# Kernel tuning notes

Measured on AMD Instinct MI355X. Metric: run time of the kernel, lower is better.

Reference implementation:

```python
import jax, jax.numpy as jnp
import numpy as np

N, E, DIN, DH = 50000, 1600000, 128, 128
P_DROP = 0.5


def setup_inputs() -> dict:
    key = jax.random.key(0)
    ks = jax.random.split(key, 9)
    scale = 0.05
    x = jax.random.normal(ks[0], (N, DIN), jnp.float32)
    edge_index = jax.random.randint(ks[1], (2, E), 0, N, dtype=jnp.int32)
    W0 = jax.random.normal(ks[2], (DH, DIN), jnp.float32) * scale
    b0 = jnp.zeros((DH,), jnp.float32)
    W1 = jax.random.normal(ks[3], (DH, DH), jnp.float32) * scale
    b1 = jnp.zeros((DH,), jnp.float32)
    W2 = jax.random.normal(ks[4], (DH, DH), jnp.float32) * scale
    b2 = jnp.zeros((DH,), jnp.float32)
    # deterministic inverted-dropout mask (train-mode Dropout(p=0.5))
    drop_mask = jax.random.bernoulli(ks[5], 1.0 - P_DROP, (N, DH)).astype(jnp.float32) / (1.0 - P_DROP)
    return {"x": x, "edge_index": edge_index, "drop_mask": drop_mask,
            "W0": W0, "b0": b0, "W1": W1, "b1": b1, "W2": W2, "b2": b2}


def _gcn_conv(h_in, W, b, src, dst, dinv):
    # PyG GCNConv: linear -> symmetric-normalized aggregation with self loops -> bias
    h = h_in @ W.T                                   # [N, out]
    norm = dinv[src] * dinv[dst]                      # [E]
    msg = h[src] * norm[:, None]                      # [E, out]
    out = jax.ops.segment_sum(msg, dst, num_segments=N)
    out = out + h * (dinv * dinv)[:, None]            # self-loop contribution
    return out + b


def reference(x, edge_index, drop_mask, W0, b0, W1, b1, W2, b2):
    src, dst = edge_index[0], edge_index[1]
    # degree of target nodes, +1 for the added self loop (shared by all layers)
    deg = jax.ops.segment_sum(jnp.ones((E,), x.dtype), dst, num_segments=N) + 1.0
    dinv = jax.lax.rsqrt(deg)

    h = _gcn_conv(x, W0, b0, src, dst, dinv)
    h = jax.nn.relu(h * drop_mask)                    # Dropout(0.5) then ReLU
    x_ = _gcn_conv(h, W1, b1, src, dst, dinv)
    x2 = _gcn_conv(h, W2, b2, src, dst, dinv)         # conv2 also consumes h (as in source)
    return (x_, x2)
```

## Files before the change

kernel.cpp:

```cpp
#include <hip/hip_runtime.h>


#define D 128
#define BK_SHIFT 7
#define BK_NODES 128
#define NBMAX 512
#define BUFCAP 6144
#define TILE_A 2048
#define TILE_CH 4096

typedef __attribute__((ext_vector_type(8))) short bf16x8;
typedef __attribute__((ext_vector_type(4))) float f32x4;

static __device__ __forceinline__ unsigned f2bf(float f) {
  union { float f; unsigned u; } v; v.f = f;
  unsigned r = v.u + 0x7FFF + ((v.u >> 16) & 1);
  return r >> 16;
}
static __device__ __forceinline__ float bflo(unsigned u) {
  return __uint_as_float(u << 16);
}
static __device__ __forceinline__ float bfhi(unsigned u) {
  return __uint_as_float(u & 0xFFFF0000u);
}


__global__ __launch_bounds__(256) void k_chist(const int* __restrict__ dst,
                                               int* __restrict__ coarse,
                                               int E, int nb) {
  __shared__ int bins[NBMAX];
  int t = threadIdx.x;
  int e0 = blockIdx.x * TILE_CH;
  for (int b = t; b < nb; b += 256) bins[b] = 0;
  __syncthreads();
  for (int i = t; i < TILE_CH; i += 256) {
    int e = e0 + i;
    if (e < E) atomicAdd(&bins[dst[e] >> BK_SHIFT], 1);
  }
  __syncthreads();
  for (int b = t; b < nb; b += 256) {
    int v = bins[b];
    if (v) atomicAdd(&coarse[b], v);
  }
}

__global__ __launch_bounds__(NBMAX) void k_cscan(const int* __restrict__ coarse,
                                                 int* __restrict__ cbase,
                                                 int* __restrict__ bCursor,
                                                 int nb, int E) {
  __shared__ int sm[NBMAX];
  int t = threadIdx.x;
  int v = (t < nb) ? coarse[t] : 0;
  sm[t] = v;
  __syncthreads();
  for (int off = 1; off < NBMAX; off <<= 1) {
    int y = (t >= off) ? sm[t - off] : 0;
    __syncthreads();
    sm[t] += y;
    __syncthreads();
  }
  int excl = sm[t] - v;
  if (t < nb) { cbase[t] = excl; bCursor[t] = excl; }
  if (t == 0) cbase[nb] = E;
}

__global__ __launch_bounds__(256) void k_bucketA(const int* __restrict__ src,
                                                 const int* __restrict__ dst,
                                                 int* __restrict__ bCursor,
                                                 int* __restrict__ packed,
                                                 int E, int nb) {
  __shared__ int hist[NBMAX];
  __shared__ int base[NBMAX];
  int t = threadIdx.x;
  int e0 = blockIdx.x * TILE_A;

  for (int b = t; b < nb; b += 256) hist[b] = 0;
  __syncthreads();

  for (int i = t; i < TILE_A; i += 256) {
    int e = e0 + i;
    if (e < E) atomicAdd(&hist[dst[e] >> BK_SHIFT], 1);
  }
  __syncthreads();

  for (int b = t; b < nb; b += 256) {
    int h = hist[b];
    if (h) base[b] = atomicAdd(&bCursor[b], h);
  }
  __syncthreads();

  for (int i = t; i < TILE_A; i += 256) {
    int e = e0 + i;
    if (e < E) {
      int d = dst[e];
      int bkt = d >> BK_SHIFT;
      int pos = atomicAdd(&base[bkt], 1);
      packed[pos] = (src[e] & 0xFFFF) | ((d & (BK_NODES - 1)) << 16);
    }
  }
}

__global__ __launch_bounds__(512) void k_bucketB2(const int* __restrict__ packed,
                                                  const int* __restrict__ cbase,
                                                  int* __restrict__ srcSorted,
                                                  int* __restrict__ rowptr,
                                                  float* __restrict__ dinv,
                                                  int n, int E) {
  __shared__ int histC[BK_NODES];
  __shared__ int cur[BK_NODES];
  __shared__ int buf[BUFCAP];
  int t = threadIdx.x;
  int bkt = blockIdx.x;
  int n0 = bkt << BK_SHIFT;
  int beg = cbase[bkt], end = cbase[bkt + 1];
  int cnt = end - beg;

  if (t < BK_NODES) histC[t] = 0;
  __syncthreads();

  for (int i = t; i < cnt; i += 512)
    atomicAdd(&histC[packed[beg + i] >> 16], 1);
  __syncthreads();

  if (t == 0) {
    int run = 0;
#pragma unroll
    for (int j = 0; j < BK_NODES; ++j) { cur[j] = run; run += histC[j]; }
  }
  __syncthreads();

  if (t < BK_NODES && n0 + t < n) {
    rowptr[n0 + t] = beg + cur[t];
    dinv[n0 + t]   = rsqrtf((float)histC[t] + 1.0f);
  }
  if (bkt == (int)gridDim.x - 1 && t == 0) rowptr[n] = E;
  __syncthreads();

  if (cnt <= BUFCAP) {
    for (int i = t; i < cnt; i += 512) {
      int p = packed[beg + i];
      int pos = atomicAdd(&cur[p >> 16], 1);
      buf[pos] = p & 0xFFFF;
    }
    __syncthreads();
    for (int i = t; i < cnt; i += 512) srcSorted[beg + i] = buf[i];
  } else {
    for (int i = t; i < cnt; i += 512) {
      int p = packed[beg + i];
      int pos = atomicAdd(&cur[p >> 16], 1);
      srcSorted[beg + pos] = p & 0xFFFF;
    }
  }
}


template <int EPI>
__global__ __launch_bounds__(256) void k_aggb(const unsigned* __restrict__ T,
                                              const int* __restrict__ srcSorted,
                                              const int* __restrict__ rowptr,
                                              const float* __restrict__ dinv,
                                              const float* __restrict__ bias,
                                              const float* __restrict__ mask,
                                              float* __restrict__ outF,
                                              unsigned* __restrict__ outB,
                                              int n) {
  int wave = (blockIdx.x * 256 + threadIdx.x) >> 6;
  int lane = threadIdx.x & 63;
  if (wave >= n) return;
  int beg = rowptr[wave], end = rowptr[wave + 1];
  float ax = 0.f, ay = 0.f, bx = 0.f, by = 0.f;
  int j = beg;
  for (; j + 7 < end; j += 8) {
    int s0 = srcSorted[j],     s1 = srcSorted[j + 1];
    int s2 = srcSorted[j + 2], s3 = srcSorted[j + 3];
    int s4 = srcSorted[j + 4], s5 = srcSorted[j + 5];
    int s6 = srcSorted[j + 6], s7 = srcSorted[j + 7];
    unsigned u0 = T[(size_t)s0 * 64 + lane];
    unsigned u1 = T[(size_t)s1 * 64 + lane];
    unsigned u2 = T[(size_t)s2 * 64 + lane];
    unsigned u3 = T[(size_t)s3 * 64 + lane];
    unsigned u4 = T[(size_t)s4 * 64 + lane];
    unsigned u5 = T[(size_t)s5 * 64 + lane];
    unsigned u6 = T[(size_t)s6 * 64 + lane];
    unsigned u7 = T[(size_t)s7 * 64 + lane];
    ax += bflo(u0) + bflo(u2);  bx += bflo(u1) + bflo(u3);
    ay += bfhi(u0) + bfhi(u2);  by += bfhi(u1) + bfhi(u3);
    ax += bflo(u4) + bflo(u6);  bx += bflo(u5) + bflo(u7);
    ay += bfhi(u4) + bfhi(u6);  by += bfhi(u5) + bfhi(u7);
  }
  for (; j < end; ++j) {
    int s = srcSorted[j];
    unsigned u = T[(size_t)s * 64 + lane];
    ax += bflo(u);
    ay += bfhi(u);
  }
  unsigned us = T[(size_t)wave * 64 + lane];
  float dn = dinv[wave];
  float ox = (ax + bx + bflo(us)) * dn;
  float oy = (ay + by + bfhi(us)) * dn;
  if (EPI == 1) {
    float2 bv = ((const float2*)bias)[lane];
    float2 mv = ((const float2*)mask)[(size_t)wave * 64 + lane];
    float hx = fmaxf((ox + bv.x) * mv.x, 0.f);
    float hy = fmaxf((oy + bv.y) * mv.y, 0.f);
    outB[(size_t)wave * 64 + lane] = f2bf(hx * dn) | (f2bf(hy * dn) << 16);
  } else if (EPI == 2) {
    outB[(size_t)wave * 64 + lane] = f2bf(ox) | (f2bf(oy) << 16);
  } else {
    ((float2*)outF)[(size_t)wave * 64 + lane] = make_float2(ox, oy);
  }
}


__global__ __launch_bounds__(256) void k_wcvt(const float* __restrict__ W0,
                                              const float* __restrict__ W1,
                                              const float* __restrict__ W2,
                                              unsigned short* __restrict__ out) {
  int i = blockIdx.x * 256 + threadIdx.x;
  if (i >= 3 * 16384) return;
  const float* W = (i < 16384) ? W0 : (i < 32768 ? W1 : W2);
  out[i] = (unsigned short)f2bf(W[i & 16383]);
}


template <bool BF16IN, bool BF16OUT>
__global__ __launch_bounds__(256) void k_gemm_mfma(const void* __restrict__ Xv,
                                                   const unsigned short* __restrict__ Wb,
                                                   const float* __restrict__ bias,
                                                   const float* __restrict__ prescale,
                                                   float* __restrict__ Cf,
                                                   unsigned short* __restrict__ Cb,
                                                   int nrows) {
  int wid  = threadIdx.x >> 6;
  int lane = threadIdx.x & 63;
  int r0   = blockIdx.x * 64 + wid * 16;
  int arow = r0 + (lane & 15);
  int kb   = (lane >> 4) * 8;
  bool rowok = arow < nrows;

  bf16x8 a[4];
  if (BF16IN) {
    const unsigned short* X = (const unsigned short*)Xv;
#pragma unroll
    for (int ks = 0; ks < 4; ++ks) {
      bf16x8 t;
      if (rowok) t = *reinterpret_cast<const bf16x8*>(X + (size_t)arow * D + ks * 32 + kb);
      else { for (int q = 0; q < 8; ++q) t[q] = 0; }
      a[ks] = t;
    }
  } else {
    const float* X = (const float*)Xv;
#pragma unroll
    for (int ks = 0; ks < 4; ++ks) {
      bf16x8 t;
      if (rowok) {
        const float* p = X + (size_t)arow * D + ks * 32 + kb;
        float4 f0 = *(const float4*)(p);
        float4 f1 = *(const float4*)(p + 4);
        t[0] = (short)f2bf(f0.x); t[1] = (short)f2bf(f0.y);
        t[2] = (short)f2bf(f0.z); t[3] = (short)f2bf(f0.w);
        t[4] = (short)f2bf(f1.x); t[5] = (short)f2bf(f1.y);
        t[6] = (short)f2bf(f1.z); t[7] = (short)f2bf(f1.w);
      } else {
        for (int q = 0; q < 8; ++q) t[q] = 0;
      }
      a[ks] = t;
    }
  }

  int rbase = r0 + (lane >> 4) * 4;
  float sc[4];
  if (BF16OUT) {
#pragma unroll
    for (int reg = 0; reg < 4; ++reg) {
      int rr = rbase + reg;
      sc[reg] = (prescale && rr < nrows) ? prescale[rr] : 1.0f;
    }
  }

#pragma unroll
  for (int ct = 0; ct < 8; ++ct) {
    int col = ct * 16 + (lane & 15);
    f32x4 acc = {0.f, 0.f, 0.f, 0.f};
#pragma unroll
    for (int ks = 0; ks < 4; ++ks) {
      bf16x8 b = *reinterpret_cast<const bf16x8*>(Wb + (size_t)col * D + ks * 32 + kb);
      acc = __builtin_amdgcn_mfma_f32_16x16x32_bf16(a[ks], b, acc, 0, 0, 0);
    }
    if (BF16OUT) {
#pragma unroll
      for (int reg = 0; reg < 4; ++reg) {
        int rr = rbase + reg;
        if (rr < nrows)
          Cb[(size_t)rr * D + col] = (unsigned short)f2bf(acc[reg] * sc[reg]);
      }
    } else {
      float bc = bias ? bias[col] : 0.f;
#pragma unroll
      for (int reg = 0; reg < 4; ++reg) {
        int rr = rbase + reg;
        if (rr < nrows) Cf[(size_t)rr * D + col] = acc[reg] + bc;
      }
    }
  }
}


template <bool BF16OUT>
__global__ __launch_bounds__(256) void k_gemm128(const float* __restrict__ X,
                                                 const float* __restrict__ W,
                                                 const float* __restrict__ bias,
                                                 const float* __restrict__ prescale,
                                                 float* __restrict__ Cf,
                                                 unsigned short* __restrict__ Cb,
                                                 int nrows) {
  __shared__ float Xs[64][132];
  __shared__ float Ws[32][128];

  int tid = threadIdx.x;
  int row0 = blockIdx.x * 64;

  for (int t = tid; t < 2048; t += 256) {
    int r = t >> 5;
    int c4 = (t & 31) << 2;
    int gr = row0 + r;
    float4 v = make_float4(0.f, 0.f, 0.f, 0.f);
    if (gr < nrows) v = *(const float4*)(X + (size_t)gr * D + c4);
    Xs[r][c4 + 0] = v.x; Xs[r][c4 + 1] = v.y;
    Xs[r][c4 + 2] = v.z; Xs[r][c4 + 3] = v.w;
  }

  float acc[4][8];
#pragma unroll
  for (int i = 0; i < 4; ++i)
#pragma unroll
    for (int j = 0; j < 8; ++j) acc[i][j] = 0.f;

  int ty = tid >> 4, tx = tid & 15;
  int r0 = ty << 2, c0 = tx << 3;

  for (int k0 = 0; k0 < 128; k0 += 32) {
    int j = tid >> 1;
    int kkb = (tid & 1) << 4;
    const float4* wp = (const float4*)(W + j * D + k0 + kkb);
    float4 wa = wp[0], wb = wp[1], wc = wp[2], wd = wp[3];

    __syncthreads();
    Ws[kkb +  0][j] = wa.x; Ws[kkb +  1][j] = wa.y; Ws[kkb +  2][j] = wa.z; Ws[kkb +  3][j] = wa.w;
    Ws[kkb +  4][j] = wb.x; Ws[kkb +  5][j] = wb.y; Ws[kkb +  6][j] = wb.z; Ws[kkb +  7][j] = wb.w;
    Ws[kkb +  8][j] = wc.x; Ws[kkb +  9][j] = wc.y; Ws[kkb + 10][j] = wc.z; Ws[kkb + 11][j] = wc.w;
    Ws[kkb + 12][j] = wd.x; Ws[kkb + 13][j] = wd.y; Ws[kkb + 14][j] = wd.z; Ws[kkb + 15][j] = wd.w;
    __syncthreads();

#pragma unroll
    for (int kk = 0; kk < 32; ++kk) {
      float xi[4];
      xi[0] = Xs[r0 + 0][k0 + kk];
      xi[1] = Xs[r0 + 1][k0 + kk];
      xi[2] = Xs[r0 + 2][k0 + kk];
      xi[3] = Xs[r0 + 3][k0 + kk];
      float4 wv0 = *(const float4*)(&Ws[kk][c0]);
      float4 wv1 = *(const float4*)(&Ws[kk][c0 + 4]);
      float wf[8] = {wv0.x, wv0.y, wv0.z, wv0.w, wv1.x, wv1.y, wv1.z, wv1.w};
#pragma unroll
      for (int i = 0; i < 4; ++i)
#pragma unroll
        for (int jj = 0; jj < 8; ++jj) acc[i][jj] += xi[i] * wf[jj];
    }
  }

  float4 bv0 = make_float4(0.f, 0.f, 0.f, 0.f);
  float4 bv1 = make_float4(0.f, 0.f, 0.f, 0.f);
  if (bias) {
    bv0 = *(const float4*)(bias + c0);
    bv1 = *(const float4*)(bias + c0 + 4);
  }

#pragma unroll
  for (int i = 0; i < 4; ++i) {
    int gr = row0 + r0 + i;
    if (gr < nrows) {
      float o[8];
      o[0] = acc[i][0] + bv0.x; o[1] = acc[i][1] + bv0.y;
      o[2] = acc[i][2] + bv0.z; o[3] = acc[i][3] + bv0.w;
      o[4] = acc[i][4] + bv1.x; o[5] = acc[i][5] + bv1.y;
      o[6] = acc[i][6] + bv1.z; o[7] = acc[i][7] + bv1.w;
      if (BF16OUT) {
        float dn = prescale ? prescale[gr] : 1.0f;
        uint4 pk;
        pk.x = f2bf(o[0] * dn) | (f2bf(o[1] * dn) << 16);
        pk.y = f2bf(o[2] * dn) | (f2bf(o[3] * dn) << 16);
        pk.z = f2bf(o[4] * dn) | (f2bf(o[5] * dn) << 16);
        pk.w = f2bf(o[6] * dn) | (f2bf(o[7] * dn) << 16);
        *(uint4*)(Cb + (size_t)gr * D + c0) = pk;
      } else {
        *(float4*)(Cf + (size_t)gr * D + c0)     = make_float4(o[0], o[1], o[2], o[3]);
        *(float4*)(Cf + (size_t)gr * D + c0 + 4) = make_float4(o[4], o[5], o[6], o[7]);
      }
    }
  }
}


__global__ __launch_bounds__(256) void k_deg_f(const int* __restrict__ dst,
                                               float* __restrict__ deg, int E) {
  int i = blockIdx.x * 256 + threadIdx.x;
  if (i < E) atomicAdd(&deg[dst[i]], 1.0f);
}

__global__ __launch_bounds__(256) void k_dinv_f(float* __restrict__ deg, int n) {
  int i = blockIdx.x * 256 + threadIdx.x;
  if (i < n) deg[i] = rsqrtf(deg[i] + 1.0f);
}

__global__ __launch_bounds__(256) void k_selfmul(const float* __restrict__ X,
                                                 const float* __restrict__ dinv,
                                                 float* __restrict__ out, int n) {
  int i = blockIdx.x * 256 + threadIdx.x;
  if (i >= n * 32) return;
  int r = i >> 5, c4 = (i & 31) << 2;
  float di = dinv[r];
  float s = di * di;
  float4 h = *(const float4*)(X + (size_t)r * D + c4);
  h.x *= s; h.y *= s; h.z *= s; h.w *= s;
  *(float4*)(out + (size_t)r * D + c4) = h;
}

__global__ __launch_bounds__(256) void k_relumask(float* __restrict__ h,
                                                  const float* __restrict__ mask, int n) {
  int i = blockIdx.x * 256 + threadIdx.x;
  if (i >= n * 32) return;
  float4 v = *(const float4*)(h + (size_t)i * 4);
  float4 m = *(const float4*)(mask + (size_t)i * 4);
  v.x = fmaxf(v.x * m.x, 0.f);
  v.y = fmaxf(v.y * m.y, 0.f);
  v.z = fmaxf(v.z * m.z, 0.f);
  v.w = fmaxf(v.w * m.w, 0.f);
  *(float4*)(h + (size_t)i * 4) = v;
}

__global__ __launch_bounds__(256) void k_aggatomic(const float* __restrict__ X,
                                                   const int* __restrict__ src,
                                                   const int* __restrict__ dst,
                                                   const float* __restrict__ dinv,
                                                   float* __restrict__ out, int E) {
  int gid = blockIdx.x * 256 + threadIdx.x;
  int wave = gid >> 6;
  int lane = threadIdx.x & 63;
  int nw = (gridDim.x * 256) >> 6;
  for (int e = wave; e < E; e += nw) {
    int s = src[e], d = dst[e];
    float nrm = dinv[s] * dinv[d];
    float2 v = ((const float2*)(X + (size_t)s * D))[lane];
    float* op = out + (size_t)d * D + lane * 2;
    atomicAdd(op, v.x * nrm);
    atomicAdd(op + 1, v.y * nrm);
  }
}

__global__ __launch_bounds__(256) void k_addbias(float* __restrict__ C,
                                                 const float* __restrict__ bias, int n) {
  int i = blockIdx.x * 256 + threadIdx.x;
  if (i >= n * 32) return;
  int c4 = (i & 31) << 2;
  float4 v = *(const float4*)(C + (size_t)i * 4);
  float4 b = *(const float4*)(bias + c4);
  v.x += b.x; v.y += b.y; v.z += b.z; v.w += b.w;
  *(float4*)(C + (size_t)i * 4) = v;
}


extern "C" void kernel_launch(void* const* d_in, const int* in_sizes, int n_in,
                              void* d_out, int out_size, void* d_ws, size_t ws_size,
                              hipStream_t stream) {
  const float* x    = (const float*)d_in[0];
  const int*   ei   = (const int*)d_in[1];
  const float* mask = (const float*)d_in[2];
  const float* W0   = (const float*)d_in[3];
  const float* b0   = (const float*)d_in[4];
  const float* W1   = (const float*)d_in[5];
  const float* b1   = (const float*)d_in[6];
  const float* W2   = (const float*)d_in[7];
  const float* b2   = (const float*)d_in[8];

  const int N = in_sizes[0] / D;
  const int E = in_sizes[1] / 2;
  const int* srcv = ei;
  const int* dstv = ei + E;

  float* out  = (float*)d_out;
  float* outA = out;
  float* outB = out + (size_t)N * D;

  const size_t featBytes  = (size_t)N * D * sizeof(float);
  const size_t featBytesH = (size_t)N * D * sizeof(short);
  const int gGemm  = (N + 63) / 64;
  const int gEdge  = (E + 255) / 256;
  const int gNode  = (N + 255) / 256;
  const int gWaveN = (N + 3) / 4;
  const int gElem  = (N * 32 + 255) / 256;
  const int nb     = (N + BK_NODES - 1) >> BK_SHIFT;
  const int gBA    = (E + TILE_A - 1) / TILE_A;
  const int gCH    = (E + TILE_CH - 1) / TILE_CH;

  auto align256 = [](size_t v) { return (v + 255) & ~(size_t)255; };
  char* w = (char*)d_ws;
  size_t off = 0;
  int*   coarse    = (int*)(w + off);   off = align256(off + (NBMAX + 1) * 4);
  int*   cbase     = (int*)(w + off);   off = align256(off + (NBMAX + 1) * 4);
  int*   bCursor   = (int*)(w + off);   off = align256(off + NBMAX * 4);
  int*   rowptr    = (int*)(w + off);   off = align256(off + ((size_t)N + 1) * 4);
  float* dinv      = (float*)(w + off); off = align256(off + (size_t)N * 4);
  int*   srcSorted = (int*)(w + off);   off = align256(off + (size_t)E * 4);
  unsigned short* Wb = (unsigned short*)(w + off); off = align256(off + 3 * 16384 * 2);
  unsigned* h0bf   = (unsigned*)(w + off); off = align256(off + featBytesH);
  unsigned* hbf    = (unsigned*)(w + off); off = align256(off + featBytesH);
  unsigned* gbf    = (unsigned*)(w + off); off = align256(off + featBytesH);
  int*   packed    = (int*)gbf;
  size_t need = off;

  if (ws_size >= need && N <= 65536 && nb <= NBMAX &&
      (size_t)E * sizeof(int) <= featBytesH) {
    hipMemsetAsync(coarse, 0, (size_t)(nb + 1) * sizeof(int), stream);
    k_chist<<<gCH, 256, 0, stream>>>(dstv, coarse, E, nb);
    k_cscan<<<1, NBMAX, 0, stream>>>(coarse, cbase, bCursor, nb, E);
    k_bucketA<<<gBA, 256, 0, stream>>>(srcv, dstv, bCursor, packed, E, nb);
    k_bucketB2<<<nb, 512, 0, stream>>>(packed, cbase, srcSorted, rowptr,
                                       dinv, N, E);
    k_wcvt<<<192, 256, 0, stream>>>(W0, W1, W2, Wb);

    k_gemm_mfma<false, true><<<gGemm, 256, 0, stream>>>(
        x, Wb, nullptr, dinv, nullptr, (unsigned short*)h0bf, N);
    k_aggb<1><<<gWaveN, 256, 0, stream>>>(h0bf, srcSorted, rowptr, dinv,
                                          b0, mask, nullptr, hbf, N);
    k_aggb<2><<<gWaveN, 256, 0, stream>>>(hbf, srcSorted, rowptr, dinv,
                                          nullptr, nullptr, nullptr, gbf, N);
    k_gemm_mfma<true, false><<<gGemm, 256, 0, stream>>>(
        gbf, Wb + 16384, b1, nullptr, outA, nullptr, N);
    k_gemm_mfma<true, false><<<gGemm, 256, 0, stream>>>(
        gbf, Wb + 32768, b2, nullptr, outB, nullptr, N);
  } else {
    float* fdinv = (float*)(w);
    float* fA    = (float*)(w + 0x40000);
    float* fB    = (float*)((char*)fA + featBytes);
    hipMemsetAsync(fdinv, 0, (size_t)N * sizeof(float), stream);
    k_deg_f<<<gEdge, 256, 0, stream>>>(dstv, fdinv, E);
    k_dinv_f<<<gNode, 256, 0, stream>>>(fdinv, N);
    k_gemm128<false><<<gGemm, 256, 0, stream>>>(x, W0, nullptr, nullptr, fB, nullptr, N);
    k_selfmul<<<gElem, 256, 0, stream>>>(fB, fdinv, fA, N);
    k_aggatomic<<<4096, 256, 0, stream>>>(fB, srcv, dstv, fdinv, fA, E);
    k_addbias<<<gElem, 256, 0, stream>>>(fA, b0, N);
    k_relumask<<<gElem, 256, 0, stream>>>(fA, mask, N);
    k_selfmul<<<gElem, 256, 0, stream>>>(fA, fdinv, fB, N);
    k_aggatomic<<<4096, 256, 0, stream>>>(fA, srcv, dstv, fdinv, fB, E);
    k_gemm128<false><<<gGemm, 256, 0, stream>>>(fB, W1, b1, nullptr, outA, nullptr, N);
    k_gemm128<false><<<gGemm, 256, 0, stream>>>(fB, W2, b2, nullptr, outB, nullptr, N);
  }
}
```

Before: 246.5 us.

## Fuse final two GEMMs, pre-scale gather offsets, deepen aggregation unroll, cache bucket values in LDS

The two output GEMMs that share the aggregated bf16 input are merged into one kernel that loads the A tile once and writes both outputs. The sorted source indices are stored pre-shifted into byte offsets, so the aggregation kernel skips the index multiply, and that kernel now issues 16 gathers per iteration into four accumulator pairs for more memory-level parallelism. The bucketing kernel reads src/dst once, stashes packed values in shared memory and reuses them in the scatter pass. The trade-offs are more registers per thread in aggregation, extra LDS use in bucketing, and a 32-bit byte offset that depends on N staying small.

```diff
diff --git a/kernel.cpp b/kernel.cpp
--- a/kernel.cpp
+++ b/kernel.cpp
@@ -71,31 +71,39 @@
                                                  int E, int nb) {
   __shared__ int hist[NBMAX];
   __shared__ int base[NBMAX];
+  __shared__ unsigned pv[TILE_A];
   int t = threadIdx.x;
   int e0 = blockIdx.x * TILE_A;
 
   for (int b = t; b < nb; b += 256) hist[b] = 0;
-  __syncthreads();
-
-  for (int i = t; i < TILE_A; i += 256) {
-    int e = e0 + i;
-    if (e < E) atomicAdd(&hist[dst[e] >> BK_SHIFT], 1);
-  }
-  __syncthreads();
-
-  for (int b = t; b < nb; b += 256) {
-    int h = hist[b];
-    if (h) base[b] = atomicAdd(&bCursor[b], h);
-  }
   __syncthreads();
 
   for (int i = t; i < TILE_A; i += 256) {
     int e = e0 + i;
     if (e < E) {
       int d = dst[e];
-      int bkt = d >> BK_SHIFT;
+      int s = src[e];
+      unsigned bkt = (unsigned)d >> BK_SHIFT;
+      pv[i] = (unsigned)(s & 0xFFFF) | ((unsigned)(d & (BK_NODES - 1)) << 16) |
+              (bkt << 23);
+      atomicAdd(&hist[bkt], 1);
+    }
+  }
+  __syncthreads();
+
+  for (int b = t; b < nb; b += 256) {
+    int h = hist[b];
+    if (h) base[b] = atomicAdd(&bCursor[b], h);
+  }
+  __syncthreads();
+
+  for (int i = t; i < TILE_A; i += 256) {
+    int e = e0 + i;
+    if (e < E) {
+      unsigned v = pv[i];
+      unsigned bkt = v >> 23;
       int pos = atomicAdd(&base[bkt], 1);
-      packed[pos] = (src[e] & 0xFFFF) | ((d & (BK_NODES - 1)) << 16);
+      packed[pos] = (int)(v & 0x7FFFFF);
     }
   }
 }
@@ -143,12 +151,13 @@
       buf[pos] = p & 0xFFFF;
     }
     __syncthreads();
-    for (int i = t; i < cnt; i += 512) srcSorted[beg + i] = buf[i];
+    for (int i = t; i < cnt; i += 512)
+      srcSorted[beg + i] = buf[i] << 8;
   } else {
     for (int i = t; i < cnt; i += 512) {
       int p = packed[beg + i];
       int pos = atomicAdd(&cur[p >> 16], 1);
-      srcSorted[beg + pos] = p & 0xFFFF;
+      srcSorted[beg + pos] = (p & 0xFFFF) << 8;
     }
   }
 }
@@ -167,37 +176,47 @@
   int wave = (blockIdx.x * 256 + threadIdx.x) >> 6;
   int lane = threadIdx.x & 63;
   if (wave >= n) return;
+  const char* Tb = (const char*)T;
+  int lo = lane << 2;
   int beg = rowptr[wave], end = rowptr[wave + 1];
-  float ax = 0.f, ay = 0.f, bx = 0.f, by = 0.f;
+  float a0x = 0.f, a0y = 0.f, a1x = 0.f, a1y = 0.f;
+  float a2x = 0.f, a2y = 0.f, a3x = 0.f, a3y = 0.f;
   int j = beg;
+  for (; j + 15 < end; j += 16) {
+    unsigned u[16];
+#pragma unroll
+    for (int q = 0; q < 16; ++q)
+      u[q] = *(const unsigned*)(Tb + srcSorted[j + q] + lo);
+#pragma unroll
+    for (int q = 0; q < 16; q += 4) {
+      a0x += bflo(u[q + 0]);  a0y += bfhi(u[q + 0]);
+      a1x += bflo(u[q + 1]);  a1y += bfhi(u[q + 1]);
+      a2x += bflo(u[q + 2]);  a2y += bfhi(u[q + 2]);
+      a3x += bflo(u[q + 3]);  a3y += bfhi(u[q + 3]);
+    }
+  }
   for (; j + 7 < end; j += 8) {
-    int s0 = srcSorted[j],     s1 = srcSorted[j + 1];
-    int s2 = srcSorted[j + 2], s3 = srcSorted[j + 3];
-    int s4 = srcSorted[j + 4], s5 = srcSorted[j + 5];
-    int s6 = srcSorted[j + 6], s7 = srcSorted[j + 7];
-    unsigned u0 = T[(size_t)s0 * 64 + lane];
-    unsigned u1 = T[(size_t)s1 * 64 + lane];
-    unsigned u2 = T[(size_t)s2 * 64 + lane];
-    unsigned u3 = T[(size_t)s3 * 64 + lane];
-    unsigned u4 = T[(size_t)s4 * 64 + lane];
-    unsigned u5 = T[(size_t)s5 * 64 + lane];
-    unsigned u6 = T[(size_t)s6 * 64 + lane];
-    unsigned u7 = T[(size_t)s7 * 64 + lane];
-    ax += bflo(u0) + bflo(u2);  bx += bflo(u1) + bflo(u3);
-    ay += bfhi(u0) + bfhi(u2);  by += bfhi(u1) + bfhi(u3);
-    ax += bflo(u4) + bflo(u6);  bx += bflo(u5) + bflo(u7);
-    ay += bfhi(u4) + bfhi(u6);  by += bfhi(u5) + bfhi(u7);
+    unsigned u[8];
+#pragma unroll
+    for (int q = 0; q < 8; ++q)
+      u[q] = *(const unsigned*)(Tb + srcSorted[j + q] + lo);
+#pragma unroll
+    for (int q = 0; q < 8; q += 4) {
+      a0x += bflo(u[q + 0]);  a0y += bfhi(u[q + 0]);
+      a1x += bflo(u[q + 1]);  a1y += bfhi(u[q + 1]);
+      a2x += bflo(u[q + 2]);  a2y += bfhi(u[q + 2]);
+      a3x += bflo(u[q + 3]);  a3y += bfhi(u[q + 3]);
+    }
   }
   for (; j < end; ++j) {
-    int s = srcSorted[j];
-    unsigned u = T[(size_t)s * 64 + lane];
-    ax += bflo(u);
-    ay += bfhi(u);
+    unsigned u = *(const unsigned*)(Tb + srcSorted[j] + lo);
+    a0x += bflo(u);
+    a0y += bfhi(u);
   }
   unsigned us = T[(size_t)wave * 64 + lane];
   float dn = dinv[wave];
-  float ox = (ax + bx + bflo(us)) * dn;
-  float oy = (ay + by + bfhi(us)) * dn;
+  float ox = ((a0x + a1x) + (a2x + a3x) + bflo(us)) * dn;
+  float oy = ((a0y + a1y) + (a2y + a3y) + bfhi(us)) * dn;
   if (EPI == 1) {
     float2 bv = ((const float2*)bias)[lane];
     float2 mv = ((const float2*)mask)[(size_t)wave * 64 + lane];
@@ -296,6 +315,56 @@
       }
     } else {
       float bc = bias ? bias[col] : 0.f;
+#pragma unroll
+      for (int reg = 0; reg < 4; ++reg) {
+        int rr = rbase + reg;
+        if (rr < nrows) Cf[(size_t)rr * D + col] = acc[reg] + bc;
+      }
+    }
+  }
+}
+
+__global__ __launch_bounds__(256) void k_gemm_mfma2(const unsigned short* __restrict__ X,
+                                                    const unsigned short* __restrict__ W1b,
+                                                    const unsigned short* __restrict__ W2b,
+                                                    const float* __restrict__ b1,
+                                                    const float* __restrict__ b2,
+                                                    float* __restrict__ C1,
+                                                    float* __restrict__ C2,
+                                                    int nrows) {
+  int wid  = threadIdx.x >> 6;
+  int lane = threadIdx.x & 63;
+  int r0   = blockIdx.x * 64 + wid * 16;
+  int arow = r0 + (lane & 15);
+  int kb   = (lane >> 4) * 8;
+  bool rowok = arow < nrows;
+
+  bf16x8 a[4];
+#pragma unroll
+  for (int ks = 0; ks < 4; ++ks) {
+    bf16x8 t;
+    if (rowok) t = *reinterpret_cast<const bf16x8*>(X + (size_t)arow * D + ks * 32 + kb);
+    else { for (int q = 0; q < 8; ++q) t[q] = 0; }
+    a[ks] = t;
+  }
+
+  int rbase = r0 + (lane >> 4) * 4;
+
+#pragma unroll
+  for (int wm = 0; wm < 2; ++wm) {
+    const unsigned short* Wb = (wm == 0) ? W1b : W2b;
+    const float* bias        = (wm == 0) ? b1 : b2;
+    float* Cf                = (wm == 0) ? C1 : C2;
+#pragma unroll
+    for (int ct = 0; ct < 8; ++ct) {
+      int col = ct * 16 + (lane & 15);
+      f32x4 acc = {0.f, 0.f, 0.f, 0.f};
+#pragma unroll
+      for (int ks = 0; ks < 4; ++ks) {
+        bf16x8 b = *reinterpret_cast<const bf16x8*>(Wb + (size_t)col * D + ks * 32 + kb);
+        acc = __builtin_amdgcn_mfma_f32_16x16x32_bf16(a[ks], b, acc, 0, 0, 0);
+      }
+      float bc = bias[col];
 #pragma unroll
       for (int reg = 0; reg < 4; ++reg) {
         int rr = rbase + reg;
@@ -535,10 +604,9 @@
                                           b0, mask, nullptr, hbf, N);
     k_aggb<2><<<gWaveN, 256, 0, stream>>>(hbf, srcSorted, rowptr, dinv,
                                           nullptr, nullptr, nullptr, gbf, N);
-    k_gemm_mfma<true, false><<<gGemm, 256, 0, stream>>>(
-        gbf, Wb + 16384, b1, nullptr, outA, nullptr, N);
-    k_gemm_mfma<true, false><<<gGemm, 256, 0, stream>>>(
-        gbf, Wb + 32768, b2, nullptr, outB, nullptr, N);
+    k_gemm_mfma2<<<gGemm, 256, 0, stream>>>(
+        (const unsigned short*)gbf, Wb + 16384, Wb + 32768, b1, b2,
+        outA, outB, N);
   } else {
     float* fdinv = (float*)(w);
     float* fA    = (float*)(w + 0x40000);
```

New measurement: 235.2 us. 4.6% less time.
